# Kernel tuning notes

Measured on AMD Instinct MI355X. Metric: run time of the kernel, lower is better.

Reference implementation:

```python
import jax, jax.numpy as jnp
import numpy as np

N_NODES = 50000
N_EDGES = 600000
FEAT = 256
HID = 128
LAYERS = 3
CLASSES = 32


def setup_inputs() -> dict:
    key = jax.random.key(0)
    ks = jax.random.split(key, 10)
    s = 0.05
    return {
        "object_features": jax.random.normal(ks[0], (N_NODES, FEAT), jnp.float32),
        "edge_index": jax.random.randint(ks[1], (2, N_EDGES), 0, N_NODES, jnp.int64),
        "emb_w": jax.random.normal(ks[2], (FEAT, HID), jnp.float32) * s,
        "emb_b": jnp.zeros((HID,), jnp.float32),
        "rel_w": jax.random.normal(ks[3], (LAYERS, HID, HID), jnp.float32) * s,
        "rel_b": jnp.zeros((LAYERS, HID), jnp.float32),
        "root_w": jax.random.normal(ks[4], (LAYERS, HID, HID), jnp.float32) * s,
        "head_w": jax.random.normal(ks[5], (2 * HID, CLASSES), jnp.float32) * s,
        "head_b": jnp.zeros((CLASSES,), jnp.float32),
    }


def reference(object_features, edge_index, emb_w, emb_b, rel_w, rel_b, root_w, head_w, head_b):
    n = object_features.shape[0]
    src, dst = edge_index[0], edge_index[1]
    # node embedding + relu
    x = jax.nn.relu(object_features @ emb_w + emb_b)  # [N, H]
    # stacked GraphConv layers: x' = relu(W_rel @ sum_{j->i} x_j + b + W_root @ x)
    for i in range(rel_w.shape[0]):
        agg = jax.ops.segment_sum(x[src], dst, num_segments=n)  # scatter-add messages
        x = jax.nn.relu(agg @ rel_w[i] + rel_b[i] + x @ root_w[i])
    # edge head: gather endpoints, concat, linear
    edge_feat = jnp.concatenate([x[src], x[dst]], axis=-1)  # [E, 2H]
    return edge_feat @ head_w + head_b  # [E, C]
```

## Files before the change

### kernel.cpp

```cpp
#include <hip/hip_runtime.h>
#include <hip/hip_bf16.h>

#define FEAT 256
#define HID 128
#define CLASSES 32
#define LAYERS 3

typedef float f4 __attribute__((ext_vector_type(4)));
typedef float f2 __attribute__((ext_vector_type(2)));
typedef __attribute__((ext_vector_type(8))) short short8;
typedef __attribute__((ext_vector_type(4))) float f32x4;
typedef unsigned int u32;
typedef __attribute__((ext_vector_type(4))) unsigned int u32x4;
typedef __attribute__((ext_vector_type(2))) unsigned int u32x2;

__device__ __forceinline__ unsigned short bf16_rne(float v) {
    unsigned u = __float_as_uint(v);
    return (unsigned short)((u + 0x7FFF + ((u >> 16) & 1)) >> 16);
}
__device__ __forceinline__ u32 bf16x2_rne(float a, float b) {
    return (u32)bf16_rne(a) | ((u32)bf16_rne(b) << 16);
}


__global__ void count_kernel(const int* __restrict__ dst, int* __restrict__ counts, int E) {
    int e = blockIdx.x * blockDim.x + threadIdx.x;
    if (e < E) atomicAdd(&counts[dst[e]], 1);
}

__global__ void partial_kernel(const int* __restrict__ counts, int* __restrict__ partials, int N) {
    int t = threadIdx.x;
    int i = blockIdx.x * 256 + t;
    int v = (i < N) ? counts[i] : 0;
#pragma unroll
    for (int off = 32; off >= 1; off >>= 1) v += __shfl_down(v, off, 64);
    __shared__ int ws[4];
    if ((t & 63) == 0) ws[t >> 6] = v;
    __syncthreads();
    if (t == 0) partials[blockIdx.x] = ws[0] + ws[1] + ws[2] + ws[3];
}

__global__ void scan_partials_kernel(const int* __restrict__ partials, int* __restrict__ poff, int NB) {
    int t = threadIdx.x, lane = t & 63, w = t >> 6;
    int v = (t < NB) ? partials[t] : 0;
    int x = v;
#pragma unroll
    for (int off = 1; off < 64; off <<= 1) {
        int y = __shfl_up(x, off, 64);
        if (lane >= off) x += y;
    }
    __shared__ int ws[4];
    if (lane == 63) ws[w] = x;
    __syncthreads();
    int woff = 0;
    for (int k = 0; k < w; ++k) woff += ws[k];
    if (t < NB) poff[t] = woff + x - v;
}

__global__ void scan_final_kernel(const int* __restrict__ counts, const int* __restrict__ poff,
                                  int* __restrict__ row_off, int* __restrict__ cursor, int N) {
    int t = threadIdx.x, lane = t & 63, w = t >> 6;
    int i = blockIdx.x * 256 + t;
    int v = (i < N) ? counts[i] : 0;
    int x = v;
#pragma unroll
    for (int off = 1; off < 64; off <<= 1) {
        int y = __shfl_up(x, off, 64);
        if (lane >= off) x += y;
    }
    __shared__ int ws[4];
    if (lane == 63) ws[w] = x;
    __syncthreads();
    int woff = 0;
    for (int k = 0; k < w; ++k) woff += ws[k];
    int excl = poff[blockIdx.x] + woff + x - v;
    if (i < N) {
        row_off[i] = excl;
        cursor[i] = excl;
        if (i == N - 1) row_off[N] = excl + v;
    }
}

__global__ void fill_kernel(const int* __restrict__ src, const int* __restrict__ dst,
                            int* __restrict__ cursor, int* __restrict__ csr_src, int E) {
    int e = blockIdx.x * blockDim.x + threadIdx.x;
    if (e < E) {
        int pos = atomicAdd(&cursor[dst[e]], 1);
        csr_src[pos] = src[e];
    }
}

__global__ void prep_emb_kernel(const float* __restrict__ emb_w, unsigned short* __restrict__ w) {
    int idx = blockIdx.x * 256 + threadIdx.x;
    if (idx >= 128 * 256) return;
    int n = idx >> 8, k = idx & 255;
    w[n * 256 + k] = bf16_rne(emb_w[k * 128 + n]);
}

__global__ void prep_layer_kernel(const float* __restrict__ rel_w, const float* __restrict__ root_w,
                                  unsigned short* __restrict__ w) {
    int idx = blockIdx.x * 256 + threadIdx.x;
    if (idx >= 3 * 128 * 256) return;
    int l = idx >> 15;
    int r = idx & 32767;
    int n = r >> 8, k = r & 255;
    float v = (k < 128) ? rel_w[l * 16384 + k * 128 + n] : root_w[l * 16384 + (k - 128) * 128 + n];
    w[idx] = bf16_rne(v);
}

__global__ void prep_head_kernel(const float* __restrict__ head_w, unsigned short* __restrict__ w) {
    int idx = blockIdx.x * 256 + threadIdx.x;
    if (idx >= 64 * 128) return;
    int c = idx >> 7, k = idx & 127;
    float v = (c < 32) ? head_w[k * 32 + c] : head_w[(128 + k) * 32 + (c - 32)];
    w[c * 128 + k] = bf16_rne(v);
}

template <int NCOL, int KTOT, bool RELU, int AFMT, bool PACKOUT>
__global__ __launch_bounds__(256) void gemm_mfma(
    const void* __restrict__ A0v, int lda0,
    const void* __restrict__ A1v, int lda1, int K0,
    const unsigned short* __restrict__ W,
    const float* __restrict__ bias, void* __restrict__ outv, int M) {
    constexpr int NCHUNK = KTOT / 32;
    constexpr int NCT = NCOL / 16;
    constexpr int CB = NCOL * 64;
    constexpr int NI = NCOL / 16;
    constexpr int NIW = NI / 4;
    constexpr int ASZ = (AFMT == 0) ? 2 : 1;

    __shared__ unsigned char lds[2][CB];

    int wv = threadIdx.x >> 6;
    int lane = threadIdx.x & 63;
    int m16 = lane & 15;
    int quad = lane >> 4;
    int rowbase = blockIdx.x * 128 + wv * 32;

    int arow[2];
#pragma unroll
    for (int rt = 0; rt < 2; ++rt) {
        int r = rowbase + rt * 16 + m16;
        arow[rt] = (r < M) ? r : (M - 1);
    }

    auto g_src = [&](int i, int kc) -> const unsigned short* {
        return W + (size_t)(i * 16 + (lane >> 2)) * KTOT + kc * 32 + (lane & 3) * 8;
    };
    auto dstoff = [&](int i) -> int { return i * 1024 + lane * 16; };
    auto aptr = [&](int kc, int rt) -> const void* {
        bool second = (kc * 32 >= K0);
        int lda = second ? lda1 : lda0;
        int kofs = kc * 32 - (second ? K0 : 0);
        if (AFMT == 0)
            return (const float*)(second ? A1v : A0v) + (size_t)arow[rt] * lda + kofs + quad * 8;
        else
            return (const unsigned short*)(second ? A1v : A0v) + (size_t)arow[rt] * lda + kofs + quad * 8;
    };

    f32x4 acc[2][NCT] = {};
    float bcol[NCT];
#pragma unroll
    for (int ct = 0; ct < NCT; ++ct) bcol[ct] = bias ? bias[ct * 16 + m16] : 0.f;

    u32x4 stg[NIW];
#pragma unroll
    for (int ii = 0; ii < NIW; ++ii) stg[ii] = *(const u32x4*)(const void*)g_src(wv * NIW + ii, 0);
    u32x4 ra[2][ASZ];
#pragma unroll
    for (int rt = 0; rt < 2; ++rt) {
        const u32x4* p = (const u32x4*)aptr(0, rt);
        ra[rt][0] = p[0];
        if (AFMT == 0) ra[rt][1] = p[1];
    }
#pragma unroll
    for (int ii = 0; ii < NIW; ++ii) *(u32x4*)(void*)(&lds[0][dstoff(wv * NIW + ii)]) = stg[ii];
    if (NCHUNK > 1) {
#pragma unroll
        for (int ii = 0; ii < NIW; ++ii) stg[ii] = *(const u32x4*)(const void*)g_src(wv * NIW + ii, 1);
    }
    __syncthreads();

#pragma unroll
    for (int kc = 0; kc < NCHUNK; ++kc) {
        int p = kc & 1;

        if (kc + 1 < NCHUNK) {
#pragma unroll
            for (int ii = 0; ii < NIW; ++ii) *(u32x4*)(void*)(&lds[p ^ 1][dstoff(wv * NIW + ii)]) = stg[ii];
            if (kc + 2 < NCHUNK) {
#pragma unroll
                for (int ii = 0; ii < NIW; ++ii) stg[ii] = *(const u32x4*)(const void*)g_src(wv * NIW + ii, kc + 2);
            }
        }

        u32x4 na[2][ASZ];
        if (kc + 1 < NCHUNK) {
#pragma unroll
            for (int rt = 0; rt < 2; ++rt) {
                const u32x4* pn = (const u32x4*)aptr(kc + 1, rt);
                na[rt][0] = pn[0];
                if (AFMT == 0) na[rt][1] = pn[1];
            }
        }

        short8 Ah[2];
#pragma unroll
        for (int rt = 0; rt < 2; ++rt) {
            if (AFMT == 0) {
                union { u32x4 u[2]; float f[8]; } cv;
                cv.u[0] = ra[rt][0];
                cv.u[1] = ra[rt][1];
#pragma unroll
                for (int j = 0; j < 8; ++j) Ah[rt][j] = (short)bf16_rne(cv.f[j]);
            } else {
                union { u32x4 u; short8 s; } cv;
                cv.u = ra[rt][0];
                Ah[rt] = cv.s;
            }
        }

#pragma unroll
        for (int ct = 0; ct < NCT; ++ct) {
            const unsigned char* ph = &lds[p][(ct * 16 + m16) * 64 + quad * 16];
            short8 Bh = *(const short8*)(const void*)ph;
#pragma unroll
            for (int rt = 0; rt < 2; ++rt)
                acc[rt][ct] = __builtin_amdgcn_mfma_f32_16x16x32_bf16(Ah[rt], Bh, acc[rt][ct], 0, 0, 0);
        }

        if (kc + 1 < NCHUNK) {
#pragma unroll
            for (int rt = 0; rt < 2; ++rt) {
                ra[rt][0] = na[rt][0];
                if (AFMT == 0) ra[rt][1] = na[rt][1];
            }
        }

        __syncthreads();
    }

#pragma unroll
    for (int rt = 0; rt < 2; ++rt) {
#pragma unroll
        for (int r = 0; r < 4; ++r) {
            int row = rowbase + rt * 16 + quad * 4 + r;
            if (row < M) {
#pragma unroll
                for (int ct = 0; ct < NCT; ++ct) {
                    float v = acc[rt][ct][r] + bcol[ct];
                    if (RELU) v = fmaxf(v, 0.f);
                    size_t idx = (size_t)row * NCOL + ct * 16 + m16;
                    if (PACKOUT) ((unsigned short*)outv)[idx] = bf16_rne(v);
                    else ((float*)outv)[idx] = v;
                }
            }
        }
    }
}

__global__ void aggregate_kernel(const u32* __restrict__ x, const int* __restrict__ row_off,
                                 const int* __restrict__ csr, u32* __restrict__ agg, int N) {
    int gw = (blockIdx.x * 256 + threadIdx.x) >> 6;
    int lane = threadIdx.x & 63;
    if (gw >= N) return;
    int beg = row_off[gw], end = row_off[gw + 1];

    f2 a0 = (f2)0.f, a1 = (f2)0.f, a2 = (f2)0.f, a3 = (f2)0.f;

    auto unp = [](u32 u) -> f2 {
        f2 r;
        r[0] = __uint_as_float(u << 16);
        r[1] = __uint_as_float(u & 0xFFFF0000u);
        return r;
    };

    int nfull = (end - beg) >> 2;
    int j = beg;
    if (nfull > 0) {
        int s0 = csr[j], s1 = csr[j + 1], s2 = csr[j + 2], s3 = csr[j + 3];
        for (int b = 1; b < nfull; ++b) {
            u32 v0 = x[(size_t)s0 * 64 + lane];
            u32 v1 = x[(size_t)s1 * 64 + lane];
            u32 v2 = x[(size_t)s2 * 64 + lane];
            u32 v3 = x[(size_t)s3 * 64 + lane];
            int jn = j + 4;
            s0 = csr[jn]; s1 = csr[jn + 1]; s2 = csr[jn + 2]; s3 = csr[jn + 3];
            a0 += unp(v0); a1 += unp(v1); a2 += unp(v2); a3 += unp(v3);
            j = jn;
        }
        u32 v0 = x[(size_t)s0 * 64 + lane];
        u32 v1 = x[(size_t)s1 * 64 + lane];
        u32 v2 = x[(size_t)s2 * 64 + lane];
        u32 v3 = x[(size_t)s3 * 64 + lane];
        a0 += unp(v0); a1 += unp(v1); a2 += unp(v2); a3 += unp(v3);
        j += 4;
    }

    int rem = end - j;
    if (rem > 0) {
        int e1 = end - 1;
        int t0 = csr[j];
        int t1 = csr[min(j + 1, e1)];
        int t2 = csr[min(j + 2, e1)];
        u32 w0 = x[(size_t)t0 * 64 + lane];
        u32 w1 = x[(size_t)t1 * 64 + lane];
        u32 w2 = x[(size_t)t2 * 64 + lane];
        a0 += unp(w0);
        if (rem > 1) a1 += unp(w1);
        if (rem > 2) a2 += unp(w2);
    }

    f2 a = (a0 + a2) + (a1 + a3);
    agg[(size_t)gw * 64 + lane] = bf16x2_rne(a[0], a[1]);
}

__global__ void edge_out_kernel(const int* __restrict__ src, const int* __restrict__ dst,
                                const float* __restrict__ pspd, const float* __restrict__ head_b,
                                float* __restrict__ out, int E) {
    int idx = blockIdx.x * blockDim.x + threadIdx.x;
    int e = idx >> 3;
    int c4 = (idx & 7) * 4;
    if (e >= E) return;
    int s = src[e], d = dst[e];
    f4 a = *(const f4*)&pspd[(size_t)s * 64 + c4];
    f4 b = *(const f4*)&pspd[(size_t)d * 64 + 32 + c4];
    f4 hb = *(const f4*)&head_b[c4];
    f4 o = a + b + hb;
    *(f4*)&out[(size_t)e * CLASSES + c4] = o;
}


extern "C" void kernel_launch(void* const* d_in, const int* in_sizes, int n_in,
                              void* d_out, int out_size, void* d_ws, size_t ws_size,
                              hipStream_t stream) {
    const float* feat   = (const float*)d_in[0];
    const int*   eidx   = (const int*)d_in[1];
    const float* emb_w  = (const float*)d_in[2];
    const float* emb_b  = (const float*)d_in[3];
    const float* rel_w  = (const float*)d_in[4];
    const float* rel_b  = (const float*)d_in[5];
    const float* root_w = (const float*)d_in[6];
    const float* head_w = (const float*)d_in[7];
    const float* head_b = (const float*)d_in[8];
    float* out = (float*)d_out;

    int N = in_sizes[0] / FEAT;
    int E = in_sizes[1] / 2;
    const int* src = eidx;
    const int* dst = eidx + E;

    u32* xA  = (u32*)d_ws;
    u32* xB  = xA + (size_t)N * 64;
    u32* agg = xB + (size_t)N * 64;
    int* counts   = (int*)(agg + (size_t)N * 64);
    int* row_off  = counts + N;
    int* cursor   = row_off + (N + 1);
    int* csr_src  = cursor + N;
    int* partials = csr_src + E;
    int* poff     = partials + 256;
    int* iend     = poff + 256;
    size_t ioff = (size_t)(iend - (int*)d_ws);
    ioff = (ioff + 3) & ~(size_t)3;
    unsigned short* we = (unsigned short*)((int*)d_ws + ioff);
    unsigned short* wl = we + 128 * 256;
    unsigned short* wp = wl + 3 * 128 * 256;

    int NB = (N + 255) / 256;

    hipMemsetAsync(counts, 0, (size_t)N * sizeof(int), stream);
    count_kernel<<<(E + 255) / 256, 256, 0, stream>>>(dst, counts, E);
    partial_kernel<<<NB, 256, 0, stream>>>(counts, partials, N);
    scan_partials_kernel<<<1, 256, 0, stream>>>(partials, poff, NB);
    scan_final_kernel<<<NB, 256, 0, stream>>>(counts, poff, row_off, cursor, N);
    fill_kernel<<<(E + 255) / 256, 256, 0, stream>>>(src, dst, cursor, csr_src, E);

    prep_emb_kernel<<<(128 * 256 + 255) / 256, 256, 0, stream>>>(emb_w, we);
    prep_layer_kernel<<<(3 * 128 * 256 + 255) / 256, 256, 0, stream>>>(rel_w, root_w, wl);
    prep_head_kernel<<<(64 * 128 + 255) / 256, 256, 0, stream>>>(head_w, wp);

    int grid = (N + 127) / 128;
    gemm_mfma<HID, FEAT, true, 0, true><<<grid, 256, 0, stream>>>(
        feat, FEAT, nullptr, 0, FEAT, we, emb_b, xA, N);

    const u32* xin = xA;
    u32* xout = xB;
    for (int l = 0; l < LAYERS; ++l) {
        aggregate_kernel<<<(N * 64 + 255) / 256, 256, 0, stream>>>(xin, row_off, csr_src, agg, N);
        gemm_mfma<HID, 2 * HID, true, 1, true><<<grid, 256, 0, stream>>>(
            agg, HID, xin, HID, HID,
            wl + (size_t)l * 128 * 256, rel_b + (size_t)l * HID, xout, N);
        u32* tmp = (u32*)xin; xin = xout; xout = tmp;
    }

    float* pspd = (float*)agg;
    gemm_mfma<64, HID, false, 1, false><<<grid, 256, 0, stream>>>(
        xin, HID, nullptr, 0, HID, wp, nullptr, pspd, N);

    edge_out_kernel<<<((size_t)E * 8 + 255) / 256, 256, 0, stream>>>(src, dst, pspd, head_b, out, E);
}
```

Baseline: 344.2 us.

## Hold weight fragments in registers and split GEMM columns across waves

The MFMA GEMM now has each wave own a quarter of the output columns and preload its whole weight slice for all K chunks into registers. This removes the LDS double-buffering and per-chunk __syncthreads. Blocks cover 64 rows instead of 128, and each wave walks four 16-row tiles, prefetching the next tile's A fragments for bf16 inputs. The three weight-prep kernels are merged into one launch. The cost is much higher register pressure (e.g. 8x8 short8 per lane for the K=256 layers), which may lower occupancy, and every wave now reloads the A rows.

Result: slower. 414.2 us (+20.3%).

```diff
diff --git a/kernel.cpp b/kernel.cpp
--- a/kernel.cpp
+++ b/kernel.cpp
@@ -12,7 +12,6 @@
 typedef __attribute__((ext_vector_type(4))) float f32x4;
 typedef unsigned int u32;
 typedef __attribute__((ext_vector_type(4))) unsigned int u32x4;
-typedef __attribute__((ext_vector_type(2))) unsigned int u32x2;
 
 __device__ __forceinline__ unsigned short bf16_rne(float v) {
     unsigned u = __float_as_uint(v);
@@ -90,30 +89,27 @@
     }
 }
 
-__global__ void prep_emb_kernel(const float* __restrict__ emb_w, unsigned short* __restrict__ w) {
+__global__ void prep_kernel(const float* __restrict__ emb_w, const float* __restrict__ rel_w,
+                            const float* __restrict__ root_w, const float* __restrict__ head_w,
+                            unsigned short* __restrict__ we, unsigned short* __restrict__ wl,
+                            unsigned short* __restrict__ wp) {
     int idx = blockIdx.x * 256 + threadIdx.x;
-    if (idx >= 128 * 256) return;
-    int n = idx >> 8, k = idx & 255;
-    w[n * 256 + k] = bf16_rne(emb_w[k * 128 + n]);
-}
-
-__global__ void prep_layer_kernel(const float* __restrict__ rel_w, const float* __restrict__ root_w,
-                                  unsigned short* __restrict__ w) {
-    int idx = blockIdx.x * 256 + threadIdx.x;
-    if (idx >= 3 * 128 * 256) return;
-    int l = idx >> 15;
-    int r = idx & 32767;
-    int n = r >> 8, k = r & 255;
-    float v = (k < 128) ? rel_w[l * 16384 + k * 128 + n] : root_w[l * 16384 + (k - 128) * 128 + n];
-    w[idx] = bf16_rne(v);
-}
-
-__global__ void prep_head_kernel(const float* __restrict__ head_w, unsigned short* __restrict__ w) {
-    int idx = blockIdx.x * 256 + threadIdx.x;
-    if (idx >= 64 * 128) return;
-    int c = idx >> 7, k = idx & 127;
-    float v = (c < 32) ? head_w[k * 32 + c] : head_w[(128 + k) * 32 + (c - 32)];
-    w[c * 128 + k] = bf16_rne(v);
+    if (idx < 128 * 256) {
+        int n = idx >> 8, k = idx & 255;
+        we[n * 256 + k] = bf16_rne(emb_w[k * 128 + n]);
+    } else if (idx < 4 * 128 * 256) {
+        int i = idx - 128 * 256;
+        int l = i >> 15;
+        int r = i & 32767;
+        int n = r >> 8, k = r & 255;
+        float v = (k < 128) ? rel_w[l * 16384 + k * 128 + n] : root_w[l * 16384 + (k - 128) * 128 + n];
+        wl[i] = bf16_rne(v);
+    } else if (idx < 4 * 128 * 256 + 64 * 128) {
+        int i = idx - 4 * 128 * 256;
+        int c = i >> 7, k = i & 127;
+        float v = (c < 32) ? head_w[k * 32 + c] : head_w[(128 + k) * 32 + (c - 32)];
+        wp[c * 128 + k] = bf16_rne(v);
+    }
 }
 
 template <int NCOL, int KTOT, bool RELU, int AFMT, bool PACKOUT>
@@ -123,134 +119,97 @@
     const unsigned short* __restrict__ W,
     const float* __restrict__ bias, void* __restrict__ outv, int M) {
     constexpr int NCHUNK = KTOT / 32;
-    constexpr int NCT = NCOL / 16;
-    constexpr int CB = NCOL * 64;
-    constexpr int NI = NCOL / 16;
-    constexpr int NIW = NI / 4;
-    constexpr int ASZ = (AFMT == 0) ? 2 : 1;
-
-    __shared__ unsigned char lds[2][CB];
+    constexpr int WCOL = NCOL / 4;
+    constexpr int NCT = WCOL / 16;
 
     int wv = threadIdx.x >> 6;
     int lane = threadIdx.x & 63;
     int m16 = lane & 15;
     int quad = lane >> 4;
-    int rowbase = blockIdx.x * 128 + wv * 32;
-
-    int arow[2];
-#pragma unroll
-    for (int rt = 0; rt < 2; ++rt) {
-        int r = rowbase + rt * 16 + m16;
-        arow[rt] = (r < M) ? r : (M - 1);
-    }
-
-    auto g_src = [&](int i, int kc) -> const unsigned short* {
-        return W + (size_t)(i * 16 + (lane >> 2)) * KTOT + kc * 32 + (lane & 3) * 8;
-    };
-    auto dstoff = [&](int i) -> int { return i * 1024 + lane * 16; };
-    auto aptr = [&](int kc, int rt) -> const void* {
+    int colbase = wv * WCOL;
+    int rowblk = blockIdx.x * 64;
+
+    short8 Bf[NCT][NCHUNK];
+#pragma unroll
+    for (int ct = 0; ct < NCT; ++ct)
+#pragma unroll
+        for (int kc = 0; kc < NCHUNK; ++kc)
+            Bf[ct][kc] = *(const short8*)(const void*)(W + (size_t)(colbase + ct * 16 + m16) * KTOT + kc * 32 + quad * 8);
+
+    float bcol[NCT];
+#pragma unroll
+    for (int ct = 0; ct < NCT; ++ct) bcol[ct] = bias ? bias[colbase + ct * 16 + m16] : 0.f;
+
+    f32x4 acc[4][NCT] = {};
+
+    auto aaddr = [&](int t, int kc) -> const void* {
+        int r = rowblk + t * 16 + m16;
+        r = (r < M) ? r : (M - 1);
         bool second = (kc * 32 >= K0);
         int lda = second ? lda1 : lda0;
         int kofs = kc * 32 - (second ? K0 : 0);
         if (AFMT == 0)
-            return (const float*)(second ? A1v : A0v) + (size_t)arow[rt] * lda + kofs + quad * 8;
+            return (const float*)(second ? A1v : A0v) + (size_t)r * lda + kofs + quad * 8;
         else
-            return (const unsigned short*)(second ? A1v : A0v) + (size_t)arow[rt] * lda + kofs + quad * 8;
+            return (const unsigned short*)(second ? A1v : A0v) + (size_t)r * lda + kofs + quad * 8;
     };
 
-    f32x4 acc[2][NCT] = {};
-    float bcol[NCT];
-#pragma unroll
-    for (int ct = 0; ct < NCT; ++ct) bcol[ct] = bias ? bias[ct * 16 + m16] : 0.f;
-
-    u32x4 stg[NIW];
-#pragma unroll
-    for (int ii = 0; ii < NIW; ++ii) stg[ii] = *(const u32x4*)(const void*)g_src(wv * NIW + ii, 0);
-    u32x4 ra[2][ASZ];
-#pragma unroll
-    for (int rt = 0; rt < 2; ++rt) {
-        const u32x4* p = (const u32x4*)aptr(0, rt);
-        ra[rt][0] = p[0];
-        if (AFMT == 0) ra[rt][1] = p[1];
-    }
-#pragma unroll
-    for (int ii = 0; ii < NIW; ++ii) *(u32x4*)(void*)(&lds[0][dstoff(wv * NIW + ii)]) = stg[ii];
-    if (NCHUNK > 1) {
-#pragma unroll
-        for (int ii = 0; ii < NIW; ++ii) stg[ii] = *(const u32x4*)(const void*)g_src(wv * NIW + ii, 1);
-    }
-    __syncthreads();
-
-#pragma unroll
-    for (int kc = 0; kc < NCHUNK; ++kc) {
-        int p = kc & 1;
-
-        if (kc + 1 < NCHUNK) {
-#pragma unroll
-            for (int ii = 0; ii < NIW; ++ii) *(u32x4*)(void*)(&lds[p ^ 1][dstoff(wv * NIW + ii)]) = stg[ii];
-            if (kc + 2 < NCHUNK) {
-#pragma unroll
-                for (int ii = 0; ii < NIW; ++ii) stg[ii] = *(const u32x4*)(const void*)g_src(wv * NIW + ii, kc + 2);
+    if (AFMT == 1) {
+        short8 Ac[NCHUNK], An[NCHUNK];
+#pragma unroll
+        for (int kc = 0; kc < NCHUNK; ++kc) Ac[kc] = *(const short8*)aaddr(0, kc);
+#pragma unroll
+        for (int t = 0; t < 4; ++t) {
+            if (t + 1 < 4) {
+#pragma unroll
+                for (int kc = 0; kc < NCHUNK; ++kc) An[kc] = *(const short8*)aaddr(t + 1, kc);
+            }
+#pragma unroll
+            for (int kc = 0; kc < NCHUNK; ++kc)
+#pragma unroll
+                for (int ct = 0; ct < NCT; ++ct)
+                    acc[t][ct] = __builtin_amdgcn_mfma_f32_16x16x32_bf16(Ac[kc], Bf[ct][kc], acc[t][ct], 0, 0, 0);
+            if (t + 1 < 4) {
+#pragma unroll
+                for (int kc = 0; kc < NCHUNK; ++kc) Ac[kc] = An[kc];
             }
         }
-
-        u32x4 na[2][ASZ];
-        if (kc + 1 < NCHUNK) {
-#pragma unroll
-            for (int rt = 0; rt < 2; ++rt) {
-                const u32x4* pn = (const u32x4*)aptr(kc + 1, rt);
-                na[rt][0] = pn[0];
-                if (AFMT == 0) na[rt][1] = pn[1];
+    } else {
+#pragma unroll
+        for (int t = 0; t < 4; ++t) {
+            u32x4 raw[NCHUNK][2];
+#pragma unroll
+            for (int kc = 0; kc < NCHUNK; ++kc) {
+                const u32x4* p = (const u32x4*)aaddr(t, kc);
+                raw[kc][0] = p[0];
+                raw[kc][1] = p[1];
+            }
+#pragma unroll
+            for (int kc = 0; kc < NCHUNK; ++kc) {
+                union { u32x4 u[2]; float f[8]; } cv;
+                cv.u[0] = raw[kc][0];
+                cv.u[1] = raw[kc][1];
+                short8 Af;
+#pragma unroll
+                for (int j = 0; j < 8; ++j) Af[j] = (short)bf16_rne(cv.f[j]);
+#pragma unroll
+                for (int ct = 0; ct < NCT; ++ct)
+                    acc[t][ct] = __builtin_amdgcn_mfma_f32_16x16x32_bf16(Af, Bf[ct][kc], acc[t][ct], 0, 0, 0);
             }
         }
-
-        short8 Ah[2];
-#pragma unroll
-        for (int rt = 0; rt < 2; ++rt) {
-            if (AFMT == 0) {
-                union { u32x4 u[2]; float f[8]; } cv;
-                cv.u[0] = ra[rt][0];
-                cv.u[1] = ra[rt][1];
-#pragma unroll
-                for (int j = 0; j < 8; ++j) Ah[rt][j] = (short)bf16_rne(cv.f[j]);
-            } else {
-                union { u32x4 u; short8 s; } cv;
-                cv.u = ra[rt][0];
-                Ah[rt] = cv.s;
-            }
-        }
-
-#pragma unroll
-        for (int ct = 0; ct < NCT; ++ct) {
-            const unsigned char* ph = &lds[p][(ct * 16 + m16) * 64 + quad * 16];
-            short8 Bh = *(const short8*)(const void*)ph;
-#pragma unroll
-            for (int rt = 0; rt < 2; ++rt)
-                acc[rt][ct] = __builtin_amdgcn_mfma_f32_16x16x32_bf16(Ah[rt], Bh, acc[rt][ct], 0, 0, 0);
-        }
-
-        if (kc + 1 < NCHUNK) {
-#pragma unroll
-            for (int rt = 0; rt < 2; ++rt) {
-                ra[rt][0] = na[rt][0];
-                if (AFMT == 0) ra[rt][1] = na[rt][1];
-            }
-        }
-
-        __syncthreads();
-    }
-
-#pragma unroll
-    for (int rt = 0; rt < 2; ++rt) {
+    }
+
+#pragma unroll
+    for (int t = 0; t < 4; ++t) {
 #pragma unroll
         for (int r = 0; r < 4; ++r) {
-            int row = rowbase + rt * 16 + quad * 4 + r;
+            int row = rowblk + t * 16 + quad * 4 + r;
             if (row < M) {
 #pragma unroll
                 for (int ct = 0; ct < NCT; ++ct) {
-                    float v = acc[rt][ct][r] + bcol[ct];
+                    float v = acc[t][ct][r] + bcol[ct];
                     if (RELU) v = fmaxf(v, 0.f);
-                    size_t idx = (size_t)row * NCOL + ct * 16 + m16;
+                    size_t idx = (size_t)row * NCOL + colbase + ct * 16 + m16;
                     if (PACKOUT) ((unsigned short*)outv)[idx] = bf16_rne(v);
                     else ((float*)outv)[idx] = v;
                 }
@@ -375,11 +334,10 @@
     scan_final_kernel<<<NB, 256, 0, stream>>>(counts, poff, row_off, cursor, N);
     fill_kernel<<<(E + 255) / 256, 256, 0, stream>>>(src, dst, cursor, csr_src, E);
 
-    prep_emb_kernel<<<(128 * 256 + 255) / 256, 256, 0, stream>>>(emb_w, we);
-    prep_layer_kernel<<<(3 * 128 * 256 + 255) / 256, 256, 0, stream>>>(rel_w, root_w, wl);
-    prep_head_kernel<<<(64 * 128 + 255) / 256, 256, 0, stream>>>(head_w, wp);
-
-    int grid = (N + 127) / 128;
+    prep_kernel<<<(4 * 128 * 256 + 64 * 128 + 255) / 256, 256, 0, stream>>>(
+        emb_w, rel_w, root_w, head_w, we, wl, wp);
+
+    int grid = (N + 63) / 64;
     gemm_mfma<HID, FEAT, true, 0, true><<<grid, 256, 0, stream>>>(
         feat, FEAT, nullptr, 0, FEAT, we, emb_b, xA, N);
 
```
